# Performance work log

Hardware: AMD Instinct MI355X
Metric: run time of the kernel (lower is better)

Reference implementation:

```python
import jax, jax.numpy as jnp
import numpy as np

B, T, K = 256, 512, 128


def setup_inputs() -> dict:
    key = jax.random.key(0)
    k1, k2, k3, k4 = jax.random.split(key, 4)
    logits = jax.random.normal(k1, (B, T, K), dtype=jnp.float32)
    labels = jax.random.randint(k2, (B, T), 0, K, dtype=jnp.int32)
    seq_lens = jax.random.randint(k3, (B,), 1, T + 1, dtype=jnp.int32)
    trans = jax.random.uniform(k4, (K, K), dtype=jnp.float32)
    return {"logits": logits, "labels": labels, "seq_lens": seq_lens, "trans": trans}


def _crf_neg_log_likelihood(logits, labels, seq_lens, trans):
    # logits: [B,T,K], labels: [B,T] int, seq_lens: [B] int, trans: [K,K]
    Bb, Tt, Kk = logits.shape
    mask = (jnp.arange(Tt)[None, :] < seq_lens[:, None])  # [B,T] bool

    # ---- gold sequence score ----
    unary = jnp.take_along_axis(logits, labels[..., None].astype(jnp.int32), axis=-1)[..., 0]  # [B,T]
    unary_score = jnp.sum(jnp.where(mask, unary, 0.0), axis=-1)  # [B]
    pair = trans[labels[:, :-1], labels[:, 1:]]  # [B,T-1]
    pair_score = jnp.sum(jnp.where(mask[:, 1:], pair, 0.0), axis=-1)  # [B]
    score = unary_score + pair_score  # [B]

    # ---- log partition via forward algorithm (lax.scan over time) ----
    alpha0 = logits[:, 0]  # [B,K]
    xs = (jnp.swapaxes(logits[:, 1:], 0, 1), jnp.swapaxes(mask[:, 1:], 0, 1))  # [T-1,B,K],[T-1,B]

    def step(alpha, x):
        logit_t, m_t = x
        # alpha[:, :, None] + trans[None] : [B, K_prev, K_next]
        new = jax.nn.logsumexp(alpha[:, :, None] + trans[None, :, :], axis=1) + logit_t
        alpha = jnp.where(m_t[:, None], new, alpha)
        return alpha, None

    alpha, _ = jax.lax.scan(step, alpha0, xs)
    log_z = jax.nn.logsumexp(alpha, axis=-1)  # [B]

    log_likelihood = score - log_z
    return jnp.sum(-log_likelihood)  # scalar, matches tf.reduce_sum(-ll)


def reference(logits, labels, seq_lens, trans):
    return _crf_neg_log_likelihood(logits, labels, seq_lens, trans)
```

## Files before the change

### kernel.cpp

```cpp
#include <hip/hip_runtime.h>

#define Bdim 256
#define Tdim 512
#define Kdim 128
#define NT   256

#define BAR() asm volatile("s_waitcnt lgkmcnt(0)\n\ts_barrier" ::: "memory")

template <int CTRL>
__device__ __forceinline__ float quad_add(float v) {
    int r = __builtin_amdgcn_update_dpp(0, __float_as_int(v), CTRL, 0xF, 0xF, true);
    return v + __int_as_float(r);
}

__global__ __launch_bounds__(NT, 1) void crf_nll_kernel(
    const float* __restrict__ logits,
    const int*   __restrict__ labels,
    const int*   __restrict__ seq_lens,
    const float* __restrict__ trans,
    float* __restrict__ out)
{
    const int b   = blockIdx.x;
    const int tid = threadIdx.x;
    const int j4  = tid >> 3;
    const int g   = tid & 7;
    const int cj  = 4 * j4 + (g & 3);
    const int L   = seq_lens[b];

    __shared__ float pbuf[2][Kdim];
    __shared__ float sred[NT / 64];
    __shared__ float ared[NT / 64];

    const int*   lab_b   = labels + (size_t)b * Tdim;
    const float* logit_b = logits + (size_t)b * Tdim * Kdim;

    float e[4][4][4];
    #pragma unroll
    for (int ii4 = 0; ii4 < 4; ++ii4) {
        const int row0 = 16 * g + (((ii4 + g) & 3) << 2);
        #pragma unroll
        for (int ci = 0; ci < 4; ++ci) {
            const float4 tr =
                *(const float4*)&trans[(size_t)(row0 + ci) * Kdim + 4 * j4];
            e[ii4][ci][0] = __expf(tr.x);
            e[ii4][ci][1] = __expf(tr.y);
            e[ii4][ci][2] = __expf(tr.z);
            e[ii4][ci][3] = __expf(tr.w);
        }
    }

    float s = 0.f;
    #pragma unroll
    for (int t0 = 0; t0 < Tdim; t0 += NT) {
        const int t = t0 + tid;
        if (t < L) {
            const int lb = lab_b[t];
            s += logit_b[(size_t)t * Kdim + lb];
            if (t >= 1) s += trans[lab_b[t - 1] * Kdim + lb];
        }
    }
    #pragma unroll
    for (int o = 32; o > 0; o >>= 1) s += __shfl_down(s, o, 64);
    if ((tid & 63) == 0) sred[tid >> 6] = s;

    float a = 0.f, off = 0.f;
    if (g < 4) {
        a = __expf(logit_b[cj]);
        pbuf[0][cj] = a;
    }
    int cb = 0;
    __syncthreads();

    float score = 0.f;
    if (tid == 0) {
        #pragma unroll
        for (int w = 0; w < NT / 64; ++w) score += sred[w];
    }

    float curl[8], nxtl[8];
    #pragma unroll
    for (int u = 0; u < 8; ++u) {
        const int tt = 1 + u;
        curl[u] = (tt < Tdim) ? logit_b[(size_t)tt * Kdim + cj] : 0.f;
    }

    for (int tb = 1; tb < L; tb += 8) {
        #pragma unroll
        for (int u = 0; u < 8; ++u) {
            const int tt = tb + 8 + u;
            nxtl[u] = (tt < Tdim) ? logit_b[(size_t)tt * Kdim + cj] : 0.f;
        }
        #pragma unroll
        for (int u = 0; u < 8; ++u) {
            const int t = tb + u;
            if (t < L) {
                const float4* p4 = (const float4*)pbuf[cb];
                const float p0 = pbuf[cb][0];
                const float lp0 = __logf(p0);
                const float sc  = __expf(curl[u] - lp0);
                float acc0 = 0.f, acc1 = 0.f, acc2 = 0.f, acc3 = 0.f;
                #pragma unroll
                for (int ii4 = 0; ii4 < 4; ++ii4) {
                    const float4 p = p4[(g << 2) + ((ii4 + g) & 3)];
                    acc0 = fmaf(p.x, e[ii4][0][0], acc0);
                    acc1 = fmaf(p.x, e[ii4][0][1], acc1);
                    acc2 = fmaf(p.x, e[ii4][0][2], acc2);
                    acc3 = fmaf(p.x, e[ii4][0][3], acc3);
                    acc0 = fmaf(p.y, e[ii4][1][0], acc0);
                    acc1 = fmaf(p.y, e[ii4][1][1], acc1);
                    acc2 = fmaf(p.y, e[ii4][1][2], acc2);
                    acc3 = fmaf(p.y, e[ii4][1][3], acc3);
                    acc0 = fmaf(p.z, e[ii4][2][0], acc0);
                    acc1 = fmaf(p.z, e[ii4][2][1], acc1);
                    acc2 = fmaf(p.z, e[ii4][2][2], acc2);
                    acc3 = fmaf(p.z, e[ii4][2][3], acc3);
                    acc0 = fmaf(p.w, e[ii4][3][0], acc0);
                    acc1 = fmaf(p.w, e[ii4][3][1], acc1);
                    acc2 = fmaf(p.w, e[ii4][3][2], acc2);
                    acc3 = fmaf(p.w, e[ii4][3][3], acc3);
                }
                off += lp0;
                acc0 = quad_add<0xB1>(acc0); acc0 = quad_add<0x4E>(acc0);
                acc1 = quad_add<0xB1>(acc1); acc1 = quad_add<0x4E>(acc1);
                acc2 = quad_add<0xB1>(acc2); acc2 = quad_add<0x4E>(acc2);
                acc3 = quad_add<0xB1>(acc3); acc3 = quad_add<0x4E>(acc3);
                float sel  = (g & 1) ? acc1 : acc0;
                float selh = (g & 1) ? acc3 : acc2;
                sel = (g & 2) ? selh : sel;
                sel += __int_as_float(__builtin_amdgcn_ds_swizzle(
                           __float_as_int(sel), 0x101F));
                const float anew = sel * sc;
                if (g < 4) {
                    a = anew;
                    pbuf[cb ^ 1][cj] = anew;
                }
                cb ^= 1;
                BAR();
            }
        }
        #pragma unroll
        for (int u = 0; u < 8; ++u) curl[u] = nxtl[u];
    }

    float as = (g < 4) ? a : 0.f;
    #pragma unroll
    for (int o = 32; o > 0; o >>= 1) as += __shfl_down(as, o, 64);
    if ((tid & 63) == 0) ared[tid >> 6] = as;
    __syncthreads();
    if (tid == 0) {
        float tot = 0.f;
        #pragma unroll
        for (int w = 0; w < NT / 64; ++w) tot += ared[w];
        const float logz = off + __logf(tot);
        atomicAdd(out, logz - score);
    }
}

extern "C" void kernel_launch(void* const* d_in, const int* in_sizes, int n_in,
                              void* d_out, int out_size, void* d_ws, size_t ws_size,
                              hipStream_t stream) {
    const float* logits   = (const float*)d_in[0];
    const int*   labels   = (const int*)d_in[1];
    const int*   seq_lens = (const int*)d_in[2];
    const float* trans    = (const float*)d_in[3];
    float* out = (float*)d_out;

    (void)hipMemsetAsync(out, 0, sizeof(float), stream);
    crf_nll_kernel<<<dim3(Bdim), dim3(NT), 0, stream>>>(
        logits, labels, seq_lens, trans, out);
}
```

Measured before the change: 274.7 us.

## Split each CRF forward step across 16 lanes with 512 threads and DPP row reduction

Doubles the block to 512 threads so each group of 16 lanes, instead of 8, shares one set of 4 output tags. Each thread now keeps half as many exponentiated transition values in registers and does half the FMAs per time step. The partial sums are combined entirely with DPP row rotates, replacing the ds_swizzle step. This shortens the per-step dependent chain in the latency-bound serial recurrence. In exchange, every step's barrier now has to synchronise 8 waves instead of 4.

Result: no change. 273.3 us (-0.5%).

```diff
diff --git a/kernel.cpp b/kernel.cpp
--- a/kernel.cpp
+++ b/kernel.cpp
@@ -3,12 +3,12 @@
 #define Bdim 256
 #define Tdim 512
 #define Kdim 128
-#define NT   256
+#define NT   512
 
 #define BAR() asm volatile("s_waitcnt lgkmcnt(0)\n\ts_barrier" ::: "memory")
 
 template <int CTRL>
-__device__ __forceinline__ float quad_add(float v) {
+__device__ __forceinline__ float dpp_add(float v) {
     int r = __builtin_amdgcn_update_dpp(0, __float_as_int(v), CTRL, 0xF, 0xF, true);
     return v + __int_as_float(r);
 }
@@ -22,8 +22,8 @@
 {
     const int b   = blockIdx.x;
     const int tid = threadIdx.x;
-    const int j4  = tid >> 3;
-    const int g   = tid & 7;
+    const int j4  = tid >> 4;
+    const int g   = tid & 15;
     const int cj  = 4 * j4 + (g & 3);
     const int L   = seq_lens[b];
 
@@ -34,28 +34,34 @@
     const int*   lab_b   = labels + (size_t)b * Tdim;
     const float* logit_b = logits + (size_t)b * Tdim * Kdim;
 
-    float e[4][4][4];
+    float e[2][4][4];
     #pragma unroll
-    for (int ii4 = 0; ii4 < 4; ++ii4) {
-        const int row0 = 16 * g + (((ii4 + g) & 3) << 2);
+    for (int ii = 0; ii < 2; ++ii) {
+        const int f = (g << 1) + (((g >> 2) & 1) ^ ii);
         #pragma unroll
         for (int ci = 0; ci < 4; ++ci) {
             const float4 tr =
-                *(const float4*)&trans[(size_t)(row0 + ci) * Kdim + 4 * j4];
-            e[ii4][ci][0] = __expf(tr.x);
-            e[ii4][ci][1] = __expf(tr.y);
-            e[ii4][ci][2] = __expf(tr.z);
-            e[ii4][ci][3] = __expf(tr.w);
+                *(const float4*)&trans[(size_t)(4 * f + ci) * Kdim + 4 * j4];
+            e[ii][ci][0] = __expf(tr.x);
+            e[ii][ci][1] = __expf(tr.y);
+            e[ii][ci][2] = __expf(tr.z);
+            e[ii][ci][3] = __expf(tr.w);
         }
     }
+    #pragma unroll
+    for (int ii = 0; ii < 2; ++ii)
+        #pragma unroll
+        for (int ci = 0; ci < 4; ++ci)
+            #pragma unroll
+            for (int c = 0; c < 4; ++c)
+                asm volatile("" : "+v"(e[ii][ci][c]));
 
     float s = 0.f;
-    #pragma unroll
-    for (int t0 = 0; t0 < Tdim; t0 += NT) {
-        const int t = t0 + tid;
+    {
+        const int t = tid;
         if (t < L) {
             const int lb = lab_b[t];
-            s += logit_b[(size_t)t * Kdim + lb];
+            s = logit_b[(size_t)t * Kdim + lb];
             if (t >= 1) s += trans[lab_b[t - 1] * Kdim + lb];
         }
     }
@@ -95,40 +101,42 @@
             const int t = tb + u;
             if (t < L) {
                 const float4* p4 = (const float4*)pbuf[cb];
-                const float p0 = pbuf[cb][0];
+                const float p0  = pbuf[cb][0];
                 const float lp0 = __logf(p0);
                 const float sc  = __expf(curl[u] - lp0);
                 float acc0 = 0.f, acc1 = 0.f, acc2 = 0.f, acc3 = 0.f;
                 #pragma unroll
-                for (int ii4 = 0; ii4 < 4; ++ii4) {
-                    const float4 p = p4[(g << 2) + ((ii4 + g) & 3)];
-                    acc0 = fmaf(p.x, e[ii4][0][0], acc0);
-                    acc1 = fmaf(p.x, e[ii4][0][1], acc1);
-                    acc2 = fmaf(p.x, e[ii4][0][2], acc2);
-                    acc3 = fmaf(p.x, e[ii4][0][3], acc3);
-                    acc0 = fmaf(p.y, e[ii4][1][0], acc0);
-                    acc1 = fmaf(p.y, e[ii4][1][1], acc1);
-                    acc2 = fmaf(p.y, e[ii4][1][2], acc2);
-                    acc3 = fmaf(p.y, e[ii4][1][3], acc3);
-                    acc0 = fmaf(p.z, e[ii4][2][0], acc0);
-                    acc1 = fmaf(p.z, e[ii4][2][1], acc1);
-                    acc2 = fmaf(p.z, e[ii4][2][2], acc2);
-                    acc3 = fmaf(p.z, e[ii4][2][3], acc3);
-                    acc0 = fmaf(p.w, e[ii4][3][0], acc0);
-                    acc1 = fmaf(p.w, e[ii4][3][1], acc1);
-                    acc2 = fmaf(p.w, e[ii4][3][2], acc2);
-                    acc3 = fmaf(p.w, e[ii4][3][3], acc3);
+                for (int ii = 0; ii < 2; ++ii) {
+                    const float4 p = p4[(g << 1) + (((g >> 2) & 1) ^ ii)];
+                    acc0 = fmaf(p.x, e[ii][0][0], acc0);
+                    acc1 = fmaf(p.x, e[ii][0][1], acc1);
+                    acc2 = fmaf(p.x, e[ii][0][2], acc2);
+                    acc3 = fmaf(p.x, e[ii][0][3], acc3);
+                    acc0 = fmaf(p.y, e[ii][1][0], acc0);
+                    acc1 = fmaf(p.y, e[ii][1][1], acc1);
+                    acc2 = fmaf(p.y, e[ii][1][2], acc2);
+                    acc3 = fmaf(p.y, e[ii][1][3], acc3);
+                    acc0 = fmaf(p.z, e[ii][2][0], acc0);
+                    acc1 = fmaf(p.z, e[ii][2][1], acc1);
+                    acc2 = fmaf(p.z, e[ii][2][2], acc2);
+                    acc3 = fmaf(p.z, e[ii][2][3], acc3);
+                    acc0 = fmaf(p.w, e[ii][3][0], acc0);
+                    acc1 = fmaf(p.w, e[ii][3][1], acc1);
+                    acc2 = fmaf(p.w, e[ii][3][2], acc2);
+                    acc3 = fmaf(p.w, e[ii][3][3], acc3);
                 }
                 off += lp0;
-                acc0 = quad_add<0xB1>(acc0); acc0 = quad_add<0x4E>(acc0);
-                acc1 = quad_add<0xB1>(acc1); acc1 = quad_add<0x4E>(acc1);
-                acc2 = quad_add<0xB1>(acc2); acc2 = quad_add<0x4E>(acc2);
-                acc3 = quad_add<0xB1>(acc3); acc3 = quad_add<0x4E>(acc3);
+                acc0 = dpp_add<0xB1>(acc0); acc0 = dpp_add<0x4E>(acc0);
+                acc0 = dpp_add<0x124>(acc0); acc0 = dpp_add<0x128>(acc0);
+                acc1 = dpp_add<0xB1>(acc1); acc1 = dpp_add<0x4E>(acc1);
+                acc1 = dpp_add<0x124>(acc1); acc1 = dpp_add<0x128>(acc1);
+                acc2 = dpp_add<0xB1>(acc2); acc2 = dpp_add<0x4E>(acc2);
+                acc2 = dpp_add<0x124>(acc2); acc2 = dpp_add<0x128>(acc2);
+                acc3 = dpp_add<0xB1>(acc3); acc3 = dpp_add<0x4E>(acc3);
+                acc3 = dpp_add<0x124>(acc3); acc3 = dpp_add<0x128>(acc3);
                 float sel  = (g & 1) ? acc1 : acc0;
                 float selh = (g & 1) ? acc3 : acc2;
                 sel = (g & 2) ? selh : sel;
-                sel += __int_as_float(__builtin_amdgcn_ds_swizzle(
-                           __float_as_int(sel), 0x101F));
                 const float anew = sel * sc;
                 if (g < 4) {
                     a = anew;
```

## Use packed FMAs, DPP reduction and periodic renormalization in CRF forward recursion

Applied to the files above, without the earlier changes.

The forward recursion now renormalizes alpha only every fourth step instead of taking log/exp of pbuf[0] at every step. It also precomputes exp(logits) for each chunk outside the dependent chain and accumulates with packed two-wide float FMAs. The ds_swizzle cross-quad add is replaced by a DPP half-row-mirror add, keeping the reduction in VALU. The goal is a shorter per-timestep serial latency between barriers, at the cost of a wider dynamic range in the unnormalized alphas, which risks overflow for extreme transition or logit values.

New measurement: 247.3 us. -10.0%, faster.

```diff
diff --git a/kernel.cpp b/kernel.cpp
--- a/kernel.cpp
+++ b/kernel.cpp
@@ -4,16 +4,20 @@
 #define Tdim 512
 #define Kdim 128
 #define NT   256
+#define CHUNK 8
+
+typedef float v2f __attribute__((ext_vector_type(2)));
 
 #define BAR() asm volatile("s_waitcnt lgkmcnt(0)\n\ts_barrier" ::: "memory")
 
 template <int CTRL>
-__device__ __forceinline__ float quad_add(float v) {
+__device__ __forceinline__ float dpp_add(float v) {
     int r = __builtin_amdgcn_update_dpp(0, __float_as_int(v), CTRL, 0xF, 0xF, true);
     return v + __int_as_float(r);
 }
 
-__global__ __launch_bounds__(NT, 1) void crf_nll_kernel(
+__global__ __launch_bounds__(NT, 1) __attribute__((amdgpu_waves_per_eu(1, 1)))
+void crf_nll_kernel(
     const float* __restrict__ logits,
     const int*   __restrict__ labels,
     const int*   __restrict__ seq_lens,
@@ -29,23 +33,20 @@
 
     __shared__ float pbuf[2][Kdim];
     __shared__ float sred[NT / 64];
-    __shared__ float ared[NT / 64];
 
     const int*   lab_b   = labels + (size_t)b * Tdim;
     const float* logit_b = logits + (size_t)b * Tdim * Kdim;
 
-    float e[4][4][4];
+    v2f e01[4][4], e23[4][4];
     #pragma unroll
-    for (int ii4 = 0; ii4 < 4; ++ii4) {
-        const int row0 = 16 * g + (((ii4 + g) & 3) << 2);
+    for (int ii = 0; ii < 4; ++ii) {
+        const int row0 = 16 * g + (((ii + g) & 3) << 2);
         #pragma unroll
         for (int ci = 0; ci < 4; ++ci) {
             const float4 tr =
                 *(const float4*)&trans[(size_t)(row0 + ci) * Kdim + 4 * j4];
-            e[ii4][ci][0] = __expf(tr.x);
-            e[ii4][ci][1] = __expf(tr.y);
-            e[ii4][ci][2] = __expf(tr.z);
-            e[ii4][ci][3] = __expf(tr.w);
+            e01[ii][ci] = (v2f){__expf(tr.x), __expf(tr.y)};
+            e23[ii][ci] = (v2f){__expf(tr.z), __expf(tr.w)};
         }
     }
 
@@ -56,18 +57,15 @@
         if (t < L) {
             const int lb = lab_b[t];
             s += logit_b[(size_t)t * Kdim + lb];
-            if (t >= 1) s += trans[lab_b[t - 1] * Kdim + lb];
+            if (t >= 1) s += trans[(size_t)lab_b[t - 1] * Kdim + lb];
         }
     }
     #pragma unroll
     for (int o = 32; o > 0; o >>= 1) s += __shfl_down(s, o, 64);
     if ((tid & 63) == 0) sred[tid >> 6] = s;
 
-    float a = 0.f, off = 0.f;
-    if (g < 4) {
-        a = __expf(logit_b[cj]);
-        pbuf[0][cj] = a;
-    }
+    if (g < 4) pbuf[0][cj] = __expf(logit_b[cj]);
+    float off = 0.f;
     int cb = 0;
     __syncthreads();
 
@@ -77,80 +75,79 @@
         for (int w = 0; w < NT / 64; ++w) score += sred[w];
     }
 
-    float curl[8], nxtl[8];
+    float curl[CHUNK], nxtl[CHUNK], ex[CHUNK];
     #pragma unroll
-    for (int u = 0; u < 8; ++u) {
+    for (int u = 0; u < CHUNK; ++u) {
         const int tt = 1 + u;
         curl[u] = (tt < Tdim) ? logit_b[(size_t)tt * Kdim + cj] : 0.f;
     }
 
-    for (int tb = 1; tb < L; tb += 8) {
+    for (int tb = 1; tb < L; tb += CHUNK) {
         #pragma unroll
-        for (int u = 0; u < 8; ++u) {
-            const int tt = tb + 8 + u;
+        for (int u = 0; u < CHUNK; ++u) {
+            const int tt = tb + CHUNK + u;
             nxtl[u] = (tt < Tdim) ? logit_b[(size_t)tt * Kdim + cj] : 0.f;
         }
         #pragma unroll
-        for (int u = 0; u < 8; ++u) {
+        for (int u = 0; u < CHUNK; ++u)
+            ex[u] = __expf(curl[u]);
+        #pragma unroll
+        for (int u = 0; u < CHUNK; ++u) {
             const int t = tb + u;
             if (t < L) {
-                const float4* p4 = (const float4*)pbuf[cb];
-                const float p0 = pbuf[cb][0];
-                const float lp0 = __logf(p0);
-                const float sc  = __expf(curl[u] - lp0);
-                float acc0 = 0.f, acc1 = 0.f, acc2 = 0.f, acc3 = 0.f;
+                const float4* a4 = (const float4*)pbuf[cb];
+                float p0 = 1.f;
+                if ((u & 3) == 3) p0 = pbuf[cb][0];
+                v2f A0 = {0.f, 0.f}, A1 = {0.f, 0.f};
+                v2f B0 = {0.f, 0.f}, B1 = {0.f, 0.f};
                 #pragma unroll
-                for (int ii4 = 0; ii4 < 4; ++ii4) {
-                    const float4 p = p4[(g << 2) + ((ii4 + g) & 3)];
-                    acc0 = fmaf(p.x, e[ii4][0][0], acc0);
-                    acc1 = fmaf(p.x, e[ii4][0][1], acc1);
-                    acc2 = fmaf(p.x, e[ii4][0][2], acc2);
-                    acc3 = fmaf(p.x, e[ii4][0][3], acc3);
-                    acc0 = fmaf(p.y, e[ii4][1][0], acc0);
-                    acc1 = fmaf(p.y, e[ii4][1][1], acc1);
-                    acc2 = fmaf(p.y, e[ii4][1][2], acc2);
-                    acc3 = fmaf(p.y, e[ii4][1][3], acc3);
-                    acc0 = fmaf(p.z, e[ii4][2][0], acc0);
-                    acc1 = fmaf(p.z, e[ii4][2][1], acc1);
-                    acc2 = fmaf(p.z, e[ii4][2][2], acc2);
-                    acc3 = fmaf(p.z, e[ii4][2][3], acc3);
-                    acc0 = fmaf(p.w, e[ii4][3][0], acc0);
-                    acc1 = fmaf(p.w, e[ii4][3][1], acc1);
-                    acc2 = fmaf(p.w, e[ii4][3][2], acc2);
-                    acc3 = fmaf(p.w, e[ii4][3][3], acc3);
+                for (int ii = 0; ii < 4; ++ii) {
+                    const float4 p = a4[(g << 2) + ((ii + g) & 3)];
+                    A0 = __builtin_elementwise_fma((v2f){p.x, p.x}, e01[ii][0], A0);
+                    A1 = __builtin_elementwise_fma((v2f){p.x, p.x}, e23[ii][0], A1);
+                    B0 = __builtin_elementwise_fma((v2f){p.y, p.y}, e01[ii][1], B0);
+                    B1 = __builtin_elementwise_fma((v2f){p.y, p.y}, e23[ii][1], B1);
+                    A0 = __builtin_elementwise_fma((v2f){p.z, p.z}, e01[ii][2], A0);
+                    A1 = __builtin_elementwise_fma((v2f){p.z, p.z}, e23[ii][2], A1);
+                    B0 = __builtin_elementwise_fma((v2f){p.w, p.w}, e01[ii][3], B0);
+                    B1 = __builtin_elementwise_fma((v2f){p.w, p.w}, e23[ii][3], B1);
                 }
-                off += lp0;
-                acc0 = quad_add<0xB1>(acc0); acc0 = quad_add<0x4E>(acc0);
-                acc1 = quad_add<0xB1>(acc1); acc1 = quad_add<0x4E>(acc1);
-                acc2 = quad_add<0xB1>(acc2); acc2 = quad_add<0x4E>(acc2);
-                acc3 = quad_add<0xB1>(acc3); acc3 = quad_add<0x4E>(acc3);
-                float sel  = (g & 1) ? acc1 : acc0;
-                float selh = (g & 1) ? acc3 : acc2;
+                const v2f s01 = A0 + B0;
+                const v2f s23 = A1 + B1;
+                float c0 = s01.x, c1 = s01.y, c2 = s23.x, c3 = s23.y;
+                c0 = dpp_add<0xB1>(c0); c0 = dpp_add<0x4E>(c0); c0 = dpp_add<0x141>(c0);
+                c1 = dpp_add<0xB1>(c1); c1 = dpp_add<0x4E>(c1); c1 = dpp_add<0x141>(c1);
+                c2 = dpp_add<0xB1>(c2); c2 = dpp_add<0x4E>(c2); c2 = dpp_add<0x141>(c2);
+                c3 = dpp_add<0xB1>(c3); c3 = dpp_add<0x4E>(c3); c3 = dpp_add<0x141>(c3);
+                float sel  = (g & 1) ? c1 : c0;
+                float selh = (g & 1) ? c3 : c2;
                 sel = (g & 2) ? selh : sel;
-                sel += __int_as_float(__builtin_amdgcn_ds_swizzle(
-                           __float_as_int(sel), 0x101F));
-                const float anew = sel * sc;
-                if (g < 4) {
-                    a = anew;
-                    pbuf[cb ^ 1][cj] = anew;
+                float anew = sel * ex[u];
+                if ((u & 3) == 3) {
+                    const float lp0 = __logf(p0);
+                    anew *= __expf(-lp0);
+                    off  += lp0;
                 }
+                if (g < 4) pbuf[cb ^ 1][cj] = anew;
                 cb ^= 1;
                 BAR();
             }
         }
         #pragma unroll
-        for (int u = 0; u < 8; ++u) curl[u] = nxtl[u];
+        for (int u = 0; u < CHUNK; ++u) curl[u] = nxtl[u];
     }
 
-    float as = (g < 4) ? a : 0.f;
+    __syncthreads();
+    float as = (tid < Kdim) ? pbuf[cb][tid] : 0.f;
     #pragma unroll
     for (int o = 32; o > 0; o >>= 1) as += __shfl_down(as, o, 64);
-    if ((tid & 63) == 0) ared[tid >> 6] = as;
+    __syncthreads();
+    if ((tid & 63) == 0) sred[tid >> 6] = as;
     __syncthreads();
     if (tid == 0) {
         float tot = 0.f;
         #pragma unroll
-        for (int w = 0; w < NT / 64; ++w) tot += ared[w];
+        for (int w = 0; w < NT / 64; ++w) tot += sred[w];
         const float logz = off + __logf(tot);
         atomicAdd(out, logz - score);
     }
```
